# Optimization experiments

Hardware: AMD Instinct MI355X
Metric: run time of the kernel (lower is better)

## Reference

```python
import jax, jax.numpy as jnp
import numpy as np

N, K, D, H = 131072, 4, 128, 128


def setup_inputs() -> dict:
    key = jax.random.key(0)
    ks = jax.random.split(key, 8)
    s = 1.0 / np.sqrt(H)  # torch default LSTM-style init scale
    return {
        "x": jax.random.normal(ks[0], (N, D), jnp.float32),
        "h_child": jax.random.normal(ks[1], (N, K, H), jnp.float32),
        "c_child": jax.random.normal(ks[2], (N, K, H), jnp.float32),
        "W_iou": jax.random.normal(ks[3], (D, 3 * H), jnp.float32) * s,
        "U_iou": jax.random.normal(ks[4], (H, 3 * H), jnp.float32) * s,
        "b_iou": jnp.zeros((3 * H,), jnp.float32),
        "W_f": jax.random.normal(ks[5], (D, H), jnp.float32) * s,
        "U_f": jax.random.normal(ks[6], (H, H), jnp.float32) * s,
        "b_f": jnp.zeros((H,), jnp.float32),
    }


def reference(x, h_child, c_child, W_iou, U_iou, b_iou, W_f, U_f, b_f):
    # Child-Sum Tree-LSTM node_forward over a batch of N nodes with K children.
    h_sum = h_child.sum(axis=1)                               # [N, H]
    iou = x @ W_iou + h_sum @ U_iou + b_iou                   # [N, 3H]
    i, o, u = jnp.split(iou, 3, axis=-1)
    i = jax.nn.sigmoid(i)
    o = jax.nn.sigmoid(o)
    u = jnp.tanh(u)
    # per-child forget gates: f_k = sigmoid(W_f x + U_f h_k + b_f)  [N, K, H]
    f = jax.nn.sigmoid((x @ W_f)[:, None, :]
                       + jnp.einsum('nkh,hg->nkg', h_child, U_f)
                       + b_f)
    c = i * u + (f * c_child).sum(axis=1)                     # [N, H]
    h = o * jnp.tanh(c)                                       # [N, H]
    return jnp.stack([h, c])                                  # [2, N, H]
```

## Files before the change

### kernel.cpp

```cpp
#include <hip/hip_runtime.h>


#define NN 131072
#define LDSS 136

typedef __attribute__((ext_vector_type(8))) short bf16x8;
typedef __attribute__((ext_vector_type(4))) float f32x4;

#define BX_HI 0
#define BX_LO 65536
#define BH_HI 131072
#define BH_LO 180224
#define UF_HI 229376
#define UF_LO 245760

__device__ __forceinline__ unsigned short f2bf(float f){
  unsigned int u = __float_as_uint(f);
  u += 0x7FFFu + ((u >> 16) & 1u);
  return (unsigned short)(u >> 16);
}
__device__ __forceinline__ float bf2f(unsigned short h){
  return __uint_as_float(((unsigned int)h) << 16);
}
__device__ __forceinline__ float sigm(float v){ return 1.f / (1.f + __expf(-v)); }
__device__ __forceinline__ float tanh_f(float v){
  float a = fabsf(v);
  float e = __expf(-2.f * a);
  float r = (1.f - e) / (1.f + e);
  return copysignf(r, v);
}

__device__ __forceinline__ void split8_store(unsigned short* hp, unsigned short* lp,
                                             const float* v){
  unsigned short h[8], l[8];
#pragma unroll
  for (int i = 0; i < 8; ++i){
    h[i] = f2bf(v[i]);
    l[i] = f2bf(v[i] - bf2f(h[i]));
  }
  uint4 uh, ul;
  uh.x = (unsigned)h[0] | ((unsigned)h[1] << 16);
  uh.y = (unsigned)h[2] | ((unsigned)h[3] << 16);
  uh.z = (unsigned)h[4] | ((unsigned)h[5] << 16);
  uh.w = (unsigned)h[6] | ((unsigned)h[7] << 16);
  ul.x = (unsigned)l[0] | ((unsigned)l[1] << 16);
  ul.y = (unsigned)l[2] | ((unsigned)l[3] << 16);
  ul.z = (unsigned)l[4] | ((unsigned)l[5] << 16);
  ul.w = (unsigned)l[6] | ((unsigned)l[7] << 16);
  *(uint4*)hp = uh;
  *(uint4*)lp = ul;
}

__global__ void prep_weights(const float* __restrict__ Wiou, const float* __restrict__ Uiou,
                             const float* __restrict__ Wf, const float* __restrict__ Uf,
                             unsigned short* __restrict__ ws){
  int tid = blockIdx.x * 256 + threadIdx.x;
  float v; int k, col, nt; unsigned int bhi, blo;
  if (tid < 65536){
    k = tid >> 9; col = tid & 511;
    v = (col < 384) ? Wiou[k * 384 + col] : Wf[k * 128 + (col - 384)];
    nt = 32; bhi = BX_HI; blo = BX_LO;
  } else if (tid < 65536 + 49152){
    int s = tid - 65536; k = s / 384; col = s - k * 384;
    v = Uiou[k * 384 + col];
    nt = 24; bhi = BH_HI; blo = BH_LO;
  } else {
    int s = tid - 65536 - 49152; k = s >> 7; col = s & 127;
    v = Uf[k * 128 + col];
    nt = 8; bhi = UF_HI; blo = UF_LO;
  }
  int kc = k >> 5, q = (k >> 3) & 3, j = k & 7;
  int nc = col >> 4, cc = col & 15;
  int lane = q * 16 + cc;
  unsigned int addr = ((unsigned)(kc * nt + nc) * 64u + (unsigned)lane) * 8u + (unsigned)j;
  unsigned short hi = f2bf(v);
  unsigned short lo = f2bf(v - bf2f(hi));
  ws[bhi + addr] = hi;
  ws[blo + addr] = lo;
}

__launch_bounds__(256, 2)
__global__ void tree_lstm_fused(const float* __restrict__ xg,
                                const float* __restrict__ hcg,
                                const float* __restrict__ ccg,
                                const float* __restrict__ b_iou,
                                const float* __restrict__ b_f,
                                const unsigned short* __restrict__ ws,
                                float* __restrict__ out){
  __shared__ alignas(16) unsigned short AxHi[32 * LDSS];
  __shared__ alignas(16) unsigned short AxLo[32 * LDSS];
  __shared__ alignas(16) unsigned short HkHi[32 * LDSS];
  __shared__ alignas(16) unsigned short HkLo[32 * LDSS];

  const int t = threadIdx.x;
  const int lane = t & 63;
  const int w = t >> 6;
  const int m = lane & 15;
  const int q = lane >> 4;
  const int node0 = blockIdx.x * 32;
  const int nc0 = 2 * w;

#pragma unroll
  for (int g = 0; g < 2; ++g){
    int idx8 = t + 256 * g;
    int row = idx8 >> 4, col8 = idx8 & 15;
    const float4* s = (const float4*)(xg + (size_t)(node0 + row) * 128 + col8 * 8);
    float4 a = s[0], b = s[1];
    float v[8] = {a.x, a.y, a.z, a.w, b.x, b.y, b.z, b.w};
    split8_store(AxHi + row * LDSS + col8 * 8, AxLo + row * LDSS + col8 * 8, v);
  }
  __syncthreads();

  const f32x4 zero = {0.f, 0.f, 0.f, 0.f};
  f32x4 acc[8][2];
#pragma unroll
  for (int c = 0; c < 8; ++c)
#pragma unroll
    for (int rt = 0; rt < 2; ++rt) acc[c][rt] = zero;

#pragma unroll
  for (int kc = 0; kc < 4; ++kc){
    bf16x8 ah[2], al[2];
#pragma unroll
    for (int rt = 0; rt < 2; ++rt){
      int off = (rt * 16 + m) * LDSS + kc * 32 + q * 8;
      ah[rt] = *(const bf16x8*)(AxHi + off);
      al[rt] = *(const bf16x8*)(AxLo + off);
    }
#pragma unroll
    for (int c = 0; c < 8; ++c){
      int nc = (c >> 1) * 8 + nc0 + (c & 1);
      bf16x8 bh = *(const bf16x8*)(ws + BX_HI + ((kc * 32 + nc) * 64 + lane) * 8);
      bf16x8 bl = *(const bf16x8*)(ws + BX_LO + ((kc * 32 + nc) * 64 + lane) * 8);
#pragma unroll
      for (int rt = 0; rt < 2; ++rt){
        acc[c][rt] = __builtin_amdgcn_mfma_f32_16x16x32_bf16(ah[rt], bh, acc[c][rt], 0, 0, 0);
        acc[c][rt] = __builtin_amdgcn_mfma_f32_16x16x32_bf16(al[rt], bh, acc[c][rt], 0, 0, 0);
        acc[c][rt] = __builtin_amdgcn_mfma_f32_16x16x32_bf16(ah[rt], bl, acc[c][rt], 0, 0, 0);
      }
    }
  }

  float hs[16];
#pragma unroll
  for (int i = 0; i < 16; ++i) hs[i] = 0.f;
  f32x4 fc[2][2];
#pragma unroll
  for (int ct = 0; ct < 2; ++ct)
#pragma unroll
    for (int rt = 0; rt < 2; ++rt) fc[ct][rt] = zero;

  float bfv[2];
#pragma unroll
  for (int ct = 0; ct < 2; ++ct) bfv[ct] = b_f[w * 32 + ct * 16 + m];

  for (int k = 0; k < 4; ++k){
    float v0[8], v1[8];
    {
      int row = t >> 4, col8 = t & 15;
      const float4* s = (const float4*)(hcg + ((size_t)(node0 + row) * 4 + k) * 128 + col8 * 8);
      float4 a = s[0], b = s[1];
      v0[0]=a.x; v0[1]=a.y; v0[2]=a.z; v0[3]=a.w; v0[4]=b.x; v0[5]=b.y; v0[6]=b.z; v0[7]=b.w;
    }
    {
      int idx8 = t + 256; int row = idx8 >> 4, col8 = idx8 & 15;
      const float4* s = (const float4*)(hcg + ((size_t)(node0 + row) * 4 + k) * 128 + col8 * 8);
      float4 a = s[0], b = s[1];
      v1[0]=a.x; v1[1]=a.y; v1[2]=a.z; v1[3]=a.w; v1[4]=b.x; v1[5]=b.y; v1[6]=b.z; v1[7]=b.w;
    }
    __syncthreads();
    {
      int row = t >> 4, col8 = t & 15;
      split8_store(HkHi + row * LDSS + col8 * 8, HkLo + row * LDSS + col8 * 8, v0);
    }
    {
      int idx8 = t + 256; int row = idx8 >> 4, col8 = idx8 & 15;
      split8_store(HkHi + row * LDSS + col8 * 8, HkLo + row * LDSS + col8 * 8, v1);
    }
#pragma unroll
    for (int i = 0; i < 8; ++i){ hs[i] += v0[i]; hs[8 + i] += v1[i]; }
    __syncthreads();

    f32x4 hu[2][2];
#pragma unroll
    for (int ct = 0; ct < 2; ++ct)
#pragma unroll
      for (int rt = 0; rt < 2; ++rt) hu[ct][rt] = zero;

#pragma unroll
    for (int kc = 0; kc < 4; ++kc){
      bf16x8 ah[2], al[2];
#pragma unroll
      for (int rt = 0; rt < 2; ++rt){
        int off = (rt * 16 + m) * LDSS + kc * 32 + q * 8;
        ah[rt] = *(const bf16x8*)(HkHi + off);
        al[rt] = *(const bf16x8*)(HkLo + off);
      }
#pragma unroll
      for (int ct = 0; ct < 2; ++ct){
        int nc = nc0 + ct;
        bf16x8 bh = *(const bf16x8*)(ws + UF_HI + ((kc * 8 + nc) * 64 + lane) * 8);
        bf16x8 bl = *(const bf16x8*)(ws + UF_LO + ((kc * 8 + nc) * 64 + lane) * 8);
#pragma unroll
        for (int rt = 0; rt < 2; ++rt){
          hu[ct][rt] = __builtin_amdgcn_mfma_f32_16x16x32_bf16(ah[rt], bh, hu[ct][rt], 0, 0, 0);
          hu[ct][rt] = __builtin_amdgcn_mfma_f32_16x16x32_bf16(al[rt], bh, hu[ct][rt], 0, 0, 0);
          hu[ct][rt] = __builtin_amdgcn_mfma_f32_16x16x32_bf16(ah[rt], bl, hu[ct][rt], 0, 0, 0);
        }
      }
    }
#pragma unroll
    for (int ct = 0; ct < 2; ++ct){
      int f = w * 32 + ct * 16 + m;
#pragma unroll
      for (int rt = 0; rt < 2; ++rt){
#pragma unroll
        for (int r = 0; r < 4; ++r){
          int node = node0 + rt * 16 + q * 4 + r;
          float pre = acc[6 + ct][rt][r] + hu[ct][rt][r] + bfv[ct];
          float fg = sigm(pre);
          float cc = ccg[((size_t)node * 4 + k) * 128 + f];
          fc[ct][rt][r] += fg * cc;
        }
      }
    }
  }

  __syncthreads();
  {
    int row = t >> 4, col8 = t & 15;
    split8_store(HkHi + row * LDSS + col8 * 8, HkLo + row * LDSS + col8 * 8, &hs[0]);
  }
  {
    int idx8 = t + 256; int row = idx8 >> 4, col8 = idx8 & 15;
    split8_store(HkHi + row * LDSS + col8 * 8, HkLo + row * LDSS + col8 * 8, &hs[8]);
  }
  __syncthreads();

#pragma unroll
  for (int kc = 0; kc < 4; ++kc){
    bf16x8 ah[2], al[2];
#pragma unroll
    for (int rt = 0; rt < 2; ++rt){
      int off = (rt * 16 + m) * LDSS + kc * 32 + q * 8;
      ah[rt] = *(const bf16x8*)(HkHi + off);
      al[rt] = *(const bf16x8*)(HkLo + off);
    }
#pragma unroll
    for (int c = 0; c < 6; ++c){
      int nc = (c >> 1) * 8 + nc0 + (c & 1);
      bf16x8 bh = *(const bf16x8*)(ws + BH_HI + ((kc * 24 + nc) * 64 + lane) * 8);
      bf16x8 bl = *(const bf16x8*)(ws + BH_LO + ((kc * 24 + nc) * 64 + lane) * 8);
#pragma unroll
      for (int rt = 0; rt < 2; ++rt){
        acc[c][rt] = __builtin_amdgcn_mfma_f32_16x16x32_bf16(ah[rt], bh, acc[c][rt], 0, 0, 0);
        acc[c][rt] = __builtin_amdgcn_mfma_f32_16x16x32_bf16(al[rt], bh, acc[c][rt], 0, 0, 0);
        acc[c][rt] = __builtin_amdgcn_mfma_f32_16x16x32_bf16(ah[rt], bl, acc[c][rt], 0, 0, 0);
      }
    }
  }

  float biv[2], bov[2], buv[2];
#pragma unroll
  for (int ct = 0; ct < 2; ++ct){
    int f = w * 32 + ct * 16 + m;
    biv[ct] = b_iou[f];
    bov[ct] = b_iou[128 + f];
    buv[ct] = b_iou[256 + f];
  }
#pragma unroll
  for (int ct = 0; ct < 2; ++ct){
    int f = w * 32 + ct * 16 + m;
#pragma unroll
    for (int rt = 0; rt < 2; ++rt){
#pragma unroll
      for (int r = 0; r < 4; ++r){
        int node = node0 + rt * 16 + q * 4 + r;
        float iv = sigm(acc[ct][rt][r] + biv[ct]);
        float ov = sigm(acc[2 + ct][rt][r] + bov[ct]);
        float uv = tanh_f(acc[4 + ct][rt][r] + buv[ct]);
        float cv = iv * uv + fc[ct][rt][r];
        float hv = ov * tanh_f(cv);
        out[(size_t)node * 128 + f] = hv;
        out[(size_t)NN * 128 + (size_t)node * 128 + f] = cv;
      }
    }
  }
}

extern "C" void kernel_launch(void* const* d_in, const int* in_sizes, int n_in,
                              void* d_out, int out_size, void* d_ws, size_t ws_size,
                              hipStream_t stream){
  const float* x       = (const float*)d_in[0];
  const float* h_child = (const float*)d_in[1];
  const float* c_child = (const float*)d_in[2];
  const float* W_iou   = (const float*)d_in[3];
  const float* U_iou   = (const float*)d_in[4];
  const float* b_iou   = (const float*)d_in[5];
  const float* W_f     = (const float*)d_in[6];
  const float* U_f     = (const float*)d_in[7];
  const float* b_f     = (const float*)d_in[8];
  unsigned short* ws   = (unsigned short*)d_ws;
  float* out           = (float*)d_out;

  prep_weights<<<512, 256, 0, stream>>>(W_iou, U_iou, W_f, U_f, ws);
  tree_lstm_fused<<<NN / 32, 256, 0, stream>>>(x, h_child, c_child, b_iou, b_f, ws, out);
}
```

Baseline: 762.9 us.

## Double-buffer child hidden tiles in LDS and prefetch next child during MFMA

Adds a second LDS buffer for child hidden states, so child k+1 is split and stored while child k's tile is consumed. The global load for child k+2 is issued ahead of time, which cuts one barrier per child and hides global latency behind the MFMAs. The change also batches the c_child loads, uses fast division in the gate activations, packs bf16 with perm instructions, raises launch-bounds occupancy to 3 blocks, and raises wave priority around the MFMA loops. The extra LDS buffer and prefetch registers may limit whether the occupancy of 3 blocks is actually reached.

```diff
diff --git a/kernel.cpp b/kernel.cpp
--- a/kernel.cpp
+++ b/kernel.cpp
@@ -22,31 +22,41 @@
 __device__ __forceinline__ float bf2f(unsigned short h){
   return __uint_as_float(((unsigned int)h) << 16);
 }
-__device__ __forceinline__ float sigm(float v){ return 1.f / (1.f + __expf(-v)); }
+__device__ __forceinline__ float sigm(float v){
+  return __fdividef(1.f, 1.f + __expf(-v));
+}
 __device__ __forceinline__ float tanh_f(float v){
   float a = fabsf(v);
   float e = __expf(-2.f * a);
-  float r = (1.f - e) / (1.f + e);
+  float r = __fdividef(1.f - e, 1.f + e);
   return copysignf(r, v);
+}
+
+__device__ __forceinline__ void load8(float* v, const float* p){
+  float4 a = ((const float4*)p)[0];
+  float4 b = ((const float4*)p)[1];
+  v[0]=a.x; v[1]=a.y; v[2]=a.z; v[3]=a.w;
+  v[4]=b.x; v[5]=b.y; v[6]=b.z; v[7]=b.w;
 }
 
 __device__ __forceinline__ void split8_store(unsigned short* hp, unsigned short* lp,
                                              const float* v){
-  unsigned short h[8], l[8];
+  unsigned int r[8]; unsigned int lo[8];
 #pragma unroll
   for (int i = 0; i < 8; ++i){
-    h[i] = f2bf(v[i]);
-    l[i] = f2bf(v[i] - bf2f(h[i]));
+    unsigned int u = __float_as_uint(v[i]);
+    r[i] = u + (0x7FFFu + ((u >> 16) & 1u));
+    lo[i] = __float_as_uint(v[i] - __uint_as_float(r[i] & 0xFFFF0000u));
   }
   uint4 uh, ul;
-  uh.x = (unsigned)h[0] | ((unsigned)h[1] << 16);
-  uh.y = (unsigned)h[2] | ((unsigned)h[3] << 16);
-  uh.z = (unsigned)h[4] | ((unsigned)h[5] << 16);
-  uh.w = (unsigned)h[6] | ((unsigned)h[7] << 16);
-  ul.x = (unsigned)l[0] | ((unsigned)l[1] << 16);
-  ul.y = (unsigned)l[2] | ((unsigned)l[3] << 16);
-  ul.z = (unsigned)l[4] | ((unsigned)l[5] << 16);
-  ul.w = (unsigned)l[6] | ((unsigned)l[7] << 16);
+  uh.x = __builtin_amdgcn_perm(r[1], r[0], 0x07060302u);
+  uh.y = __builtin_amdgcn_perm(r[3], r[2], 0x07060302u);
+  uh.z = __builtin_amdgcn_perm(r[5], r[4], 0x07060302u);
+  uh.w = __builtin_amdgcn_perm(r[7], r[6], 0x07060302u);
+  ul.x = __builtin_amdgcn_perm(lo[1], lo[0], 0x07060302u);
+  ul.y = __builtin_amdgcn_perm(lo[3], lo[2], 0x07060302u);
+  ul.z = __builtin_amdgcn_perm(lo[5], lo[4], 0x07060302u);
+  ul.w = __builtin_amdgcn_perm(lo[7], lo[6], 0x07060302u);
   *(uint4*)hp = uh;
   *(uint4*)lp = ul;
 }
@@ -79,7 +89,7 @@
   ws[blo + addr] = lo;
 }
 
-__launch_bounds__(256, 2)
+__launch_bounds__(256, 3)
 __global__ void tree_lstm_fused(const float* __restrict__ xg,
                                 const float* __restrict__ hcg,
                                 const float* __restrict__ ccg,
@@ -89,8 +99,10 @@
                                 float* __restrict__ out){
   __shared__ alignas(16) unsigned short AxHi[32 * LDSS];
   __shared__ alignas(16) unsigned short AxLo[32 * LDSS];
-  __shared__ alignas(16) unsigned short HkHi[32 * LDSS];
-  __shared__ alignas(16) unsigned short HkLo[32 * LDSS];
+  __shared__ alignas(16) unsigned short H0Hi[32 * LDSS];
+  __shared__ alignas(16) unsigned short H0Lo[32 * LDSS];
+  __shared__ alignas(16) unsigned short H1Hi[32 * LDSS];
+  __shared__ alignas(16) unsigned short H1Lo[32 * LDSS];
 
   const int t = threadIdx.x;
   const int lane = t & 63;
@@ -99,17 +111,33 @@
   const int q = lane >> 4;
   const int node0 = blockIdx.x * 32;
   const int nc0 = 2 * w;
-
-#pragma unroll
-  for (int g = 0; g < 2; ++g){
-    int idx8 = t + 256 * g;
-    int row = idx8 >> 4, col8 = idx8 & 15;
-    const float4* s = (const float4*)(xg + (size_t)(node0 + row) * 128 + col8 * 8);
-    float4 a = s[0], b = s[1];
-    float v[8] = {a.x, a.y, a.z, a.w, b.x, b.y, b.z, b.w};
-    split8_store(AxHi + row * LDSS + col8 * 8, AxLo + row * LDSS + col8 * 8, v);
-  }
+  const int row0 = t >> 4;
+  const int col8 = t & 15;
+  const int row1 = row0 + 16;
+
+  float xv0[8], xv1[8], hv0[8], hv1[8];
+  load8(xv0, xg + (size_t)(node0 + row0) * 128 + col8 * 8);
+  load8(xv1, xg + (size_t)(node0 + row1) * 128 + col8 * 8);
+  load8(hv0, hcg + ((size_t)(node0 + row0) * 4 + 0) * 128 + col8 * 8);
+  load8(hv1, hcg + ((size_t)(node0 + row1) * 4 + 0) * 128 + col8 * 8);
+
+  split8_store(AxHi + row0 * LDSS + col8 * 8, AxLo + row0 * LDSS + col8 * 8, xv0);
+  split8_store(AxHi + row1 * LDSS + col8 * 8, AxLo + row1 * LDSS + col8 * 8, xv1);
+  split8_store(H0Hi + row0 * LDSS + col8 * 8, H0Lo + row0 * LDSS + col8 * 8, hv0);
+  split8_store(H0Hi + row1 * LDSS + col8 * 8, H0Lo + row1 * LDSS + col8 * 8, hv1);
+
+  float hs0[8], hs1[8];
+#pragma unroll
+  for (int i = 0; i < 8; ++i){ hs0[i] = hv0[i]; hs1[i] = hv1[i]; }
+
+  float bfv[2];
+#pragma unroll
+  for (int ct = 0; ct < 2; ++ct) bfv[ct] = b_f[w * 32 + ct * 16 + m];
+
   __syncthreads();
+
+  load8(hv0, hcg + ((size_t)(node0 + row0) * 4 + 1) * 128 + col8 * 8);
+  load8(hv1, hcg + ((size_t)(node0 + row1) * 4 + 1) * 128 + col8 * 8);
 
   const f32x4 zero = {0.f, 0.f, 0.f, 0.f};
   f32x4 acc[8][2];
@@ -117,7 +145,13 @@
   for (int c = 0; c < 8; ++c)
 #pragma unroll
     for (int rt = 0; rt < 2; ++rt) acc[c][rt] = zero;
-
+  f32x4 fc[2][2];
+#pragma unroll
+  for (int ct = 0; ct < 2; ++ct)
+#pragma unroll
+    for (int rt = 0; rt < 2; ++rt) fc[ct][rt] = zero;
+
+  __builtin_amdgcn_s_setprio(1);
 #pragma unroll
   for (int kc = 0; kc < 4; ++kc){
     bf16x8 ah[2], al[2];
@@ -140,46 +174,12 @@
       }
     }
   }
-
-  float hs[16];
-#pragma unroll
-  for (int i = 0; i < 16; ++i) hs[i] = 0.f;
-  f32x4 fc[2][2];
-#pragma unroll
-  for (int ct = 0; ct < 2; ++ct)
-#pragma unroll
-    for (int rt = 0; rt < 2; ++rt) fc[ct][rt] = zero;
-
-  float bfv[2];
-#pragma unroll
-  for (int ct = 0; ct < 2; ++ct) bfv[ct] = b_f[w * 32 + ct * 16 + m];
-
+  __builtin_amdgcn_s_setprio(0);
+
+#pragma unroll
   for (int k = 0; k < 4; ++k){
-    float v0[8], v1[8];
-    {
-      int row = t >> 4, col8 = t & 15;
-      const float4* s = (const float4*)(hcg + ((size_t)(node0 + row) * 4 + k) * 128 + col8 * 8);
-      float4 a = s[0], b = s[1];
-      v0[0]=a.x; v0[1]=a.y; v0[2]=a.z; v0[3]=a.w; v0[4]=b.x; v0[5]=b.y; v0[6]=b.z; v0[7]=b.w;
-    }
-    {
-      int idx8 = t + 256; int row = idx8 >> 4, col8 = idx8 & 15;
-      const float4* s = (const float4*)(hcg + ((size_t)(node0 + row) * 4 + k) * 128 + col8 * 8);
-      float4 a = s[0], b = s[1];
-      v1[0]=a.x; v1[1]=a.y; v1[2]=a.z; v1[3]=a.w; v1[4]=b.x; v1[5]=b.y; v1[6]=b.z; v1[7]=b.w;
-    }
-    __syncthreads();
-    {
-      int row = t >> 4, col8 = t & 15;
-      split8_store(HkHi + row * LDSS + col8 * 8, HkLo + row * LDSS + col8 * 8, v0);
-    }
-    {
-      int idx8 = t + 256; int row = idx8 >> 4, col8 = idx8 & 15;
-      split8_store(HkHi + row * LDSS + col8 * 8, HkLo + row * LDSS + col8 * 8, v1);
-    }
-#pragma unroll
-    for (int i = 0; i < 8; ++i){ hs[i] += v0[i]; hs[8 + i] += v1[i]; }
-    __syncthreads();
+    const unsigned short* HHi = (k & 1) ? H1Hi : H0Hi;
+    const unsigned short* HLo = (k & 1) ? H1Lo : H0Lo;
 
     f32x4 hu[2][2];
 #pragma unroll
@@ -187,14 +187,15 @@
 #pragma unroll
       for (int rt = 0; rt < 2; ++rt) hu[ct][rt] = zero;
 
+    __builtin_amdgcn_s_setprio(1);
 #pragma unroll
     for (int kc = 0; kc < 4; ++kc){
       bf16x8 ah[2], al[2];
 #pragma unroll
       for (int rt = 0; rt < 2; ++rt){
         int off = (rt * 16 + m) * LDSS + kc * 32 + q * 8;
-        ah[rt] = *(const bf16x8*)(HkHi + off);
-        al[rt] = *(const bf16x8*)(HkLo + off);
+        ah[rt] = *(const bf16x8*)(HHi + off);
+        al[rt] = *(const bf16x8*)(HLo + off);
       }
 #pragma unroll
       for (int ct = 0; ct < 2; ++ct){
@@ -209,42 +210,54 @@
         }
       }
     }
-#pragma unroll
-    for (int ct = 0; ct < 2; ++ct){
-      int f = w * 32 + ct * 16 + m;
-#pragma unroll
-      for (int rt = 0; rt < 2; ++rt){
+    __builtin_amdgcn_s_setprio(0);
+
+    float cv[2][2][4];
+#pragma unroll
+    for (int ct = 0; ct < 2; ++ct)
+#pragma unroll
+      for (int rt = 0; rt < 2; ++rt)
+#pragma unroll
+        for (int r = 0; r < 4; ++r)
+          cv[ct][rt][r] = ccg[((size_t)(node0 + rt * 16 + q * 4 + r) * 4 + k) * 128
+                              + w * 32 + ct * 16 + m];
+#pragma unroll
+    for (int ct = 0; ct < 2; ++ct)
+#pragma unroll
+      for (int rt = 0; rt < 2; ++rt)
 #pragma unroll
         for (int r = 0; r < 4; ++r){
-          int node = node0 + rt * 16 + q * 4 + r;
           float pre = acc[6 + ct][rt][r] + hu[ct][rt][r] + bfv[ct];
-          float fg = sigm(pre);
-          float cc = ccg[((size_t)node * 4 + k) * 128 + f];
-          fc[ct][rt][r] += fg * cc;
+          fc[ct][rt][r] += sigm(pre) * cv[ct][rt][r];
         }
-      }
-    }
-  }
-
-  __syncthreads();
-  {
-    int row = t >> 4, col8 = t & 15;
-    split8_store(HkHi + row * LDSS + col8 * 8, HkLo + row * LDSS + col8 * 8, &hs[0]);
-  }
-  {
-    int idx8 = t + 256; int row = idx8 >> 4, col8 = idx8 & 15;
-    split8_store(HkHi + row * LDSS + col8 * 8, HkLo + row * LDSS + col8 * 8, &hs[8]);
-  }
-  __syncthreads();
-
+
+    unsigned short* WHi = ((k + 1) & 1) ? H1Hi : H0Hi;
+    unsigned short* WLo = ((k + 1) & 1) ? H1Lo : H0Lo;
+    if (k < 3){
+      split8_store(WHi + row0 * LDSS + col8 * 8, WLo + row0 * LDSS + col8 * 8, hv0);
+      split8_store(WHi + row1 * LDSS + col8 * 8, WLo + row1 * LDSS + col8 * 8, hv1);
+#pragma unroll
+      for (int i = 0; i < 8; ++i){ hs0[i] += hv0[i]; hs1[i] += hv1[i]; }
+      if (k < 2){
+        load8(hv0, hcg + ((size_t)(node0 + row0) * 4 + (k + 2)) * 128 + col8 * 8);
+        load8(hv1, hcg + ((size_t)(node0 + row1) * 4 + (k + 2)) * 128 + col8 * 8);
+      }
+    } else {
+      split8_store(WHi + row0 * LDSS + col8 * 8, WLo + row0 * LDSS + col8 * 8, hs0);
+      split8_store(WHi + row1 * LDSS + col8 * 8, WLo + row1 * LDSS + col8 * 8, hs1);
+    }
+    __syncthreads();
+  }
+
+  __builtin_amdgcn_s_setprio(1);
 #pragma unroll
   for (int kc = 0; kc < 4; ++kc){
     bf16x8 ah[2], al[2];
 #pragma unroll
     for (int rt = 0; rt < 2; ++rt){
       int off = (rt * 16 + m) * LDSS + kc * 32 + q * 8;
-      ah[rt] = *(const bf16x8*)(HkHi + off);
-      al[rt] = *(const bf16x8*)(HkLo + off);
+      ah[rt] = *(const bf16x8*)(H0Hi + off);
+      al[rt] = *(const bf16x8*)(H0Lo + off);
     }
 #pragma unroll
     for (int c = 0; c < 6; ++c){
@@ -259,6 +272,7 @@
       }
     }
   }
+  __builtin_amdgcn_s_setprio(0);
 
   float biv[2], bov[2], buv[2];
 #pragma unroll
@@ -279,10 +293,10 @@
         float iv = sigm(acc[ct][rt][r] + biv[ct]);
         float ov = sigm(acc[2 + ct][rt][r] + bov[ct]);
         float uv = tanh_f(acc[4 + ct][rt][r] + buv[ct]);
-        float cv = iv * uv + fc[ct][rt][r];
-        float hv = ov * tanh_f(cv);
-        out[(size_t)node * 128 + f] = hv;
-        out[(size_t)NN * 128 + (size_t)node * 128 + f] = cv;
+        float cvv = iv * uv + fc[ct][rt][r];
+        float hvv = ov * tanh_f(cvv);
+        out[(size_t)node * 128 + f] = hvv;
+        out[(size_t)NN * 128 + (size_t)node * 128 + f] = cvv;
       }
     }
   }
```

New measurement: 900.0 us. 1.18x slower.
